# Optimization experiments

Measured on AMD Instinct MI355X. Metric: run time of the kernel, lower is better.

The kernel has to match this reference:

```python
import jax, jax.numpy as jnp
import numpy as np

EPS = 1e-6

def _rms_norm(x, w):
    # per-head RMSNorm over last dim (head_dim)
    var = jnp.mean(jnp.square(x), axis=-1, keepdims=True)
    return x * jax.lax.rsqrt(var + EPS) * w

def _linear(x, w, b):
    # torch nn.Linear: y = x @ W^T + b
    return jnp.einsum('bsd,od->bso', x, w) + b

def setup_inputs() -> dict:
    key = jax.random.key(0)
    ks = jax.random.split(key, 16)
    B, S, S_enc, D, H, HD = 1, 2048, 256, 1536, 24, 64
    w = lambda k: jax.random.normal(k, (D, D), dtype=jnp.float32) * 0.02
    return {
        'hidden_states': jax.random.normal(ks[0], (B, S, D), dtype=jnp.float32),
        'encoder_hidden_states': jax.random.normal(ks[1], (B, S_enc, D), dtype=jnp.float32),
        'attention_mask': jnp.zeros((B, 1, 1, S + S_enc), dtype=jnp.float32),
        'to_q_weight': w(ks[2]), 'to_q_bias': jnp.zeros((D,), jnp.float32),
        'to_k_weight': w(ks[3]), 'to_k_bias': jnp.zeros((D,), jnp.float32),
        'to_v_weight': w(ks[4]), 'to_v_bias': jnp.zeros((D,), jnp.float32),
        'norm_q_weight': jnp.ones((HD,), jnp.float32),
        'norm_k_weight': jnp.ones((HD,), jnp.float32),
        'add_q_proj_weight': w(ks[5]), 'add_q_proj_bias': jnp.zeros((D,), jnp.float32),
        'add_k_proj_weight': w(ks[6]), 'add_k_proj_bias': jnp.zeros((D,), jnp.float32),
        'add_v_proj_weight': w(ks[7]), 'add_v_proj_bias': jnp.zeros((D,), jnp.float32),
        'norm_added_q_weight': jnp.ones((HD,), jnp.float32),
        'norm_added_k_weight': jnp.ones((HD,), jnp.float32),
        'to_out_0_weight': w(ks[8]), 'to_out_0_bias': jnp.zeros((D,), jnp.float32),
        'to_add_out_weight': w(ks[9]), 'to_add_out_bias': jnp.zeros((D,), jnp.float32),
        'attn_heads': 24,
        'attn_head_dim': 64,
    }

def reference(hidden_states, encoder_hidden_states, attention_mask,
              to_q_weight, to_q_bias, to_k_weight, to_k_bias, to_v_weight, to_v_bias,
              norm_q_weight, norm_k_weight,
              add_q_proj_weight, add_q_proj_bias, add_k_proj_weight, add_k_proj_bias,
              add_v_proj_weight, add_v_proj_bias,
              norm_added_q_weight, norm_added_k_weight,
              to_out_0_weight, to_out_0_bias, to_add_out_weight, to_add_out_bias,
              attn_heads, attn_head_dim):
    B, S, D = hidden_states.shape
    S_enc = encoder_hidden_states.shape[1]
    H, HD = attn_heads, attn_head_dim
    scale = float(HD) ** -0.5

    def split_heads(x):  # [B,T,H*HD] -> [B,H,T,HD]
        return x.reshape(B, -1, H, HD).transpose(0, 2, 1, 3)

    # hidden-stream QKV + per-head RMSNorm on q,k
    q = _rms_norm(split_heads(_linear(hidden_states, to_q_weight, to_q_bias)), norm_q_weight)
    k = _rms_norm(split_heads(_linear(hidden_states, to_k_weight, to_k_bias)), norm_k_weight)
    v = split_heads(_linear(hidden_states, to_v_weight, to_v_bias))

    # encoder-stream QKV + per-head RMSNorm on q,k
    eq = _rms_norm(split_heads(_linear(encoder_hidden_states, add_q_proj_weight, add_q_proj_bias)), norm_added_q_weight)
    ek = _rms_norm(split_heads(_linear(encoder_hidden_states, add_k_proj_weight, add_k_proj_bias)), norm_added_k_weight)
    ev = split_heads(_linear(encoder_hidden_states, add_v_proj_weight, add_v_proj_bias))

    # concat streams along sequence: [B,H,S+S_enc,HD]
    q = jnp.concatenate([q, eq], axis=2)
    k = jnp.concatenate([k, ek], axis=2)
    v = jnp.concatenate([v, ev], axis=2)

    # SDPA with additive mask
    scores = jnp.einsum('bhqd,bhkd->bhqk', q, k) * scale + attention_mask
    probs = jax.nn.softmax(scores, axis=-1)
    out = jnp.einsum('bhqk,bhkd->bhqd', probs, v)  # [B,H,T,HD]
    out = out.transpose(0, 2, 1, 3).reshape(B, S + S_enc, H * HD)

    # split back into image / text streams, separate output projections
    attn_output = _linear(out[:, :S], to_out_0_weight, to_out_0_bias)
    context_attn_output = _linear(out[:, S:], to_add_out_weight, to_add_out_bias)
    del context_attn_output  # AttentionFunc returns only the hidden-stream output
    return attn_output
```

## Files before the change

### kernel.cpp

```cpp
#include <hip/hip_runtime.h>
#include <cstdint>


typedef __attribute__((ext_vector_type(8))) short s16x8;
typedef __attribute__((ext_vector_type(4))) float f32x4;

#define LOG2E 1.4426950408889634f

__device__ __forceinline__ short f2bf(float f) {
  union { float f; uint32_t u; } v; v.f = f;
  uint32_t r = v.u + 0x7FFFu + ((v.u >> 16) & 1u);
  return (short)(r >> 16);
}
__device__ __forceinline__ short f2bf_fast(float f) {
  union { float f; uint32_t u; } v; v.f = f;
  return (short)((v.u + 0x8000u) >> 16);
}

typedef uint32_t __attribute__((address_space(1)))* gas_u32;
typedef uint32_t __attribute__((address_space(3)))* las_u32;

__device__ __forceinline__ void gload_lds16(const short* g, short* l) {
  __builtin_amdgcn_global_load_lds((gas_u32)(g), (las_u32)(l), 16, 0, 0);
}

struct CvtSeg { const float* src; short* dst; int n4; };
struct CvtArgs { CvtSeg s[8]; };

__global__ __launch_bounds__(256) void cvt_bf16_kernel(CvtArgs a) {
  const int stride = gridDim.x * blockDim.x;
  const int tid = blockIdx.x * blockDim.x + threadIdx.x;
  for (int i = 0; i < 8; ++i) {
    const float4* src = (const float4*)a.s[i].src;
    short* dst = a.s[i].dst;
    const int n4 = a.s[i].n4;
    for (int j = tid; j < n4; j += stride) {
      float4 v = src[j];
      short4 o;
      o.x = f2bf(v.x); o.y = f2bf(v.y); o.z = f2bf(v.z); o.w = f2bf(v.w);
      *(short4*)(dst + (size_t)j * 4) = o;
    }
  }
}

enum { MODE_Q = 0, MODE_K = 1, MODE_V = 2, MODE_OUT = 3 };

struct GemmCfg {
  const short* A;
  const short* W;
  const float* bias;
  const float* normw;
  void* dst;
  int toff;
  int mode;
  int mtiles;
};
struct GemmArgs { GemmCfg c[5]; };

__global__ __launch_bounds__(256) void proj_gemm_kernel(GemmArgs args) {
  const GemmCfg cfg = args.c[blockIdx.z];
  if ((int)blockIdx.y >= cfg.mtiles) return;
  constexpr int K = 1536;
  __shared__ short As[4096];
  __shared__ short Bs[4096];
  const int t = threadIdx.x;
  const int lane = t & 63;
  const int wave = t >> 6;
  const int l16 = lane & 15;
  const int quad = lane >> 4;
  const int wm = wave >> 1;
  const int wn = wave & 1;

  const short* __restrict__ Ag = cfg.A + (size_t)(blockIdx.y * 128) * K;
  const short* __restrict__ Wg = cfg.W + (size_t)(blockIdx.x * 128) * K;
  const int srow = t >> 2;
  const int scol = (t & 3) << 3;

  const f32x4 z4 = {0.f, 0.f, 0.f, 0.f};
  f32x4 acc[4][4];
#pragma unroll
  for (int i = 0; i < 4; ++i) {
#pragma unroll
    for (int j = 0; j < 4; ++j) acc[i][j] = z4;
  }

  for (int k0 = 0; k0 < K; k0 += 32) {
    gload_lds16(Ag + (size_t)srow * K + k0 + scol, As + t * 8);
    gload_lds16(Ag + (size_t)(srow + 64) * K + k0 + scol, As + 2048 + t * 8);
    gload_lds16(Wg + (size_t)srow * K + k0 + scol, Bs + t * 8);
    gload_lds16(Wg + (size_t)(srow + 64) * K + k0 + scol, Bs + 2048 + t * 8);
    __syncthreads();
    s16x8 af[4], bfr[4];
#pragma unroll
    for (int i = 0; i < 4; ++i)
      af[i] = *(const s16x8*)(As + (wm * 64 + i * 16 + l16) * 32 + quad * 8);
#pragma unroll
    for (int i = 0; i < 4; ++i)
      bfr[i] = *(const s16x8*)(Bs + (wn * 64 + i * 16 + l16) * 32 + quad * 8);
#pragma unroll
    for (int mi = 0; mi < 4; ++mi) {
#pragma unroll
      for (int ni = 0; ni < 4; ++ni)
        acc[mi][ni] = __builtin_amdgcn_mfma_f32_16x16x32_bf16(af[mi], bfr[ni], acc[mi][ni], 0, 0, 0);
    }
    __syncthreads();
  }

  const int nbase = blockIdx.x * 128 + wn * 64;
  const int mbase = blockIdx.y * 128 + wm * 64;
  const int mode = cfg.mode;
  const int h = nbase >> 6;

  float biasv[4], nwv[4];
#pragma unroll
  for (int ni = 0; ni < 4; ++ni) {
    int col = nbase + ni * 16 + l16;
    biasv[ni] = cfg.bias[col];
    nwv[ni] = (mode == MODE_Q || mode == MODE_K) ? cfg.normw[col & 63] : 0.f;
  }

#pragma unroll
  for (int mi = 0; mi < 4; ++mi) {
    float vv[4][4];
#pragma unroll
    for (int ni = 0; ni < 4; ++ni) {
#pragma unroll
      for (int r = 0; r < 4; ++r) vv[ni][r] = acc[mi][ni][r] + biasv[ni];
    }
    if (mode == MODE_Q || mode == MODE_K) {
      float ss[4];
#pragma unroll
      for (int r = 0; r < 4; ++r)
        ss[r] = vv[0][r] * vv[0][r] + vv[1][r] * vv[1][r] +
                vv[2][r] * vv[2][r] + vv[3][r] * vv[3][r];
#pragma unroll
      for (int r = 0; r < 4; ++r) {
        ss[r] += __shfl_xor(ss[r], 1);
        ss[r] += __shfl_xor(ss[r], 2);
        ss[r] += __shfl_xor(ss[r], 4);
        ss[r] += __shfl_xor(ss[r], 8);
        float rs = rsqrtf(ss[r] * (1.0f / 64.0f) + 1e-6f);
#pragma unroll
        for (int ni = 0; ni < 4; ++ni) vv[ni][r] *= rs * nwv[ni];
      }
    }
    const int row0 = mbase + mi * 16 + quad * 4;
    if (mode == MODE_Q) {
      short* Qd = (short*)cfg.dst;
#pragma unroll
      for (int ni = 0; ni < 4; ++ni) {
        int d = ni * 16 + l16;
#pragma unroll
        for (int r = 0; r < 4; ++r)
          Qd[((size_t)h * 2048 + row0 + r) * 64 + d] = f2bf(vv[ni][r]);
      }
    } else if (mode == MODE_K) {
      short* Kd = (short*)cfg.dst;
#pragma unroll
      for (int ni = 0; ni < 4; ++ni) {
        int d = ni * 16 + l16;
#pragma unroll
        for (int r = 0; r < 4; ++r)
          Kd[((size_t)h * 2304 + cfg.toff + row0 + r) * 64 + d] = f2bf(vv[ni][r]);
      }
    } else if (mode == MODE_V) {
      short* Vd = (short*)cfg.dst;
#pragma unroll
      for (int ni = 0; ni < 4; ++ni) {
        int d = ni * 16 + l16;
        short4 o4;
        o4.x = f2bf(vv[ni][0]); o4.y = f2bf(vv[ni][1]);
        o4.z = f2bf(vv[ni][2]); o4.w = f2bf(vv[ni][3]);
        *(short4*)(Vd + ((size_t)h * 64 + d) * 2304 + cfg.toff + row0) = o4;
      }
    } else {
      float* Od = (float*)cfg.dst;
#pragma unroll
      for (int ni = 0; ni < 4; ++ni) {
        int col = nbase + ni * 16 + l16;
#pragma unroll
        for (int r = 0; r < 4; ++r)
          Od[(size_t)(row0 + r) * 1536 + col] = vv[ni][r];
      }
    }
  }
}

__global__ __launch_bounds__(256) void flash_kernel(
    const short* __restrict__ Q, const short* __restrict__ Kc,
    const short* __restrict__ VT, const float* __restrict__ mask,
    short* __restrict__ AO) {
  const int b = blockIdx.x;
  const int h = (b & 7) * 3 + ((b >> 3) % 3);
  const int q0 = ((b >> 3) / 3) * 64;
  const int lane = threadIdx.x & 63;
  const int wave = threadIdx.x >> 6;
  const int l16 = lane & 15;
  const int quad = lane >> 4;

  __shared__ __align__(16) short smem[20480];
  short* Pw = smem + 16384 + wave * 1024;

  const short* Kh = Kc + (size_t)h * 2304 * 64;
  const short* Vh = VT + (size_t)h * 64 * 2304;

  const short* Qrow = Q + ((size_t)h * 2048 + q0 + wave * 16 + l16) * 64;
  s16x8 aq0 = *(const s16x8*)(Qrow + quad * 8);
  s16x8 aq1 = *(const s16x8*)(Qrow + quad * 8 + 32);

  s16x8 ones;
#pragma unroll
  for (int i = 0; i < 8; ++i) ones[i] = (short)0x3F80;

  const f32x4 z4 = {0.f, 0.f, 0.f, 0.f};
  f32x4 o[4] = {z4, z4, z4, z4};
  f32x4 lacc = z4;
  const float SC = 0.125f * LOG2E;

  const int srow = lane >> 3;
  const int schunk = (lane & 7) ^ srow;

  auto stage = [&](int kb, int buf) {
    const short* kg = Kh + (size_t)(kb + wave * 16) * 64;
    short* kt = smem + buf * 4096 + wave * 1024;
    gload_lds16(kg + srow * 64 + schunk * 8, kt + lane * 8);
    gload_lds16(kg + (srow + 8) * 64 + schunk * 8, kt + 512 + lane * 8);
    const short* vg = Vh + (size_t)(wave * 16 + srow) * 2304 + kb;
    short* vt = smem + 8192 + buf * 4096 + wave * 1024;
    gload_lds16(vg + schunk * 8, vt + lane * 8);
    gload_lds16(vg + (size_t)8 * 2304 + schunk * 8, vt + 512 + lane * 8);
  };

  stage(0, 0);
  __syncthreads();

  for (int it = 0; it < 36; ++it) {
    const int buf = it & 1;
    if (it < 35) stage((it + 1) * 64, buf ^ 1);
    const short* kt = smem + buf * 4096;
    const short* vt = smem + 8192 + buf * 4096;
    const int kb = it * 64;

#pragma unroll
    for (int ni = 0; ni < 4; ++ni) {
      const int r = ni * 16 + l16;
      const short* kr = kt + r * 64;
      s16x8 bk0 = *(const s16x8*)(kr + ((quad ^ (r & 7)) << 3));
      s16x8 bk1 = *(const s16x8*)(kr + (((quad + 4) ^ (r & 7)) << 3));
      f32x4 p0 = __builtin_amdgcn_mfma_f32_16x16x32_bf16(aq0, bk0, z4, 0, 0, 0);
      f32x4 s  = __builtin_amdgcn_mfma_f32_16x16x32_bf16(aq1, bk1, p0, 0, 0, 0);
      float mvl = mask[kb + r] * LOG2E;
      int cb = r >> 3;
#pragma unroll
      for (int rr = 0; rr < 4; ++rr) {
        float pv = __builtin_amdgcn_exp2f(fmaf(s[rr], SC, mvl));
        int prow = quad * 4 + rr;
        Pw[prow * 64 + ((cb ^ (prow & 7)) << 3) + (r & 7)] = f2bf_fast(pv);
      }
    }
    s16x8 ap0 = *(const s16x8*)(Pw + l16 * 64 + ((quad ^ (l16 & 7)) << 3));
    s16x8 ap1 = *(const s16x8*)(Pw + l16 * 64 + (((quad + 4) ^ (l16 & 7)) << 3));
    lacc = __builtin_amdgcn_mfma_f32_16x16x32_bf16(ap0, ones, lacc, 0, 0, 0);
    lacc = __builtin_amdgcn_mfma_f32_16x16x32_bf16(ap1, ones, lacc, 0, 0, 0);
#pragma unroll
    for (int ni = 0; ni < 4; ++ni) {
      const int r = ni * 16 + l16;
      const short* vr = vt + r * 64;
      s16x8 bv0 = *(const s16x8*)(vr + ((quad ^ (r & 7)) << 3));
      s16x8 bv1 = *(const s16x8*)(vr + (((quad + 4) ^ (r & 7)) << 3));
      o[ni] = __builtin_amdgcn_mfma_f32_16x16x32_bf16(ap0, bv0, o[ni], 0, 0, 0);
      o[ni] = __builtin_amdgcn_mfma_f32_16x16x32_bf16(ap1, bv1, o[ni], 0, 0, 0);
    }
    __syncthreads();
  }

#pragma unroll
  for (int rr = 0; rr < 4; ++rr) {
    float inv = 1.0f / lacc[rr];
    int tq = q0 + wave * 16 + quad * 4 + rr;
#pragma unroll
    for (int ni = 0; ni < 4; ++ni)
      AO[(size_t)tq * 1536 + h * 64 + ni * 16 + l16] = f2bf(o[ni][rr] * inv);
  }
}

extern "C" void kernel_launch(void* const* d_in, const int* in_sizes, int n_in,
                              void* d_out, int out_size, void* d_ws, size_t ws_size,
                              hipStream_t stream) {
  (void)in_sizes; (void)n_in; (void)out_size; (void)ws_size;
  const float* hidden = (const float*)d_in[0];
  const float* enc    = (const float*)d_in[1];
  const float* amask  = (const float*)d_in[2];
  const float* wq  = (const float*)d_in[3];  const float* bq  = (const float*)d_in[4];
  const float* wk  = (const float*)d_in[5];  const float* bk  = (const float*)d_in[6];
  const float* wv  = (const float*)d_in[7];  const float* bv  = (const float*)d_in[8];
  const float* nqw = (const float*)d_in[9];  const float* nkw = (const float*)d_in[10];
  const float* wak = (const float*)d_in[13]; const float* bak = (const float*)d_in[14];
  const float* wav = (const float*)d_in[15]; const float* bav = (const float*)d_in[16];
  const float* nakw = (const float*)d_in[18];
  const float* wo  = (const float*)d_in[19]; const float* bo  = (const float*)d_in[20];
  float* out = (float*)d_out;

  char* p = (char*)d_ws;
  auto carve = [&](size_t bytes) { char* r = p; p += (bytes + 255) & ~(size_t)255; return r; };
  short* Xb   = (short*)carve((size_t)2048 * 1536 * 2);
  short* Eb   = (short*)carve((size_t)256 * 1536 * 2);
  short* Wqb  = (short*)carve((size_t)1536 * 1536 * 2);
  short* Wkb  = (short*)carve((size_t)1536 * 1536 * 2);
  short* Wvb  = (short*)carve((size_t)1536 * 1536 * 2);
  short* Wakb = (short*)carve((size_t)1536 * 1536 * 2);
  short* Wavb = (short*)carve((size_t)1536 * 1536 * 2);
  short* Wob  = (short*)carve((size_t)1536 * 1536 * 2);
  short* Qb   = (short*)carve((size_t)24 * 2048 * 64 * 2);
  short* Kb   = (short*)carve((size_t)24 * 2304 * 64 * 2);
  short* VTb  = (short*)carve((size_t)24 * 64 * 2304 * 2);
  short* AOb  = (short*)carve((size_t)2048 * 1536 * 2);

  CvtArgs ca;
  ca.s[0] = {hidden, Xb, 2048 * 1536 / 4};
  ca.s[1] = {enc,    Eb, 256 * 1536 / 4};
  ca.s[2] = {wq,  Wqb,  1536 * 1536 / 4};
  ca.s[3] = {wk,  Wkb,  1536 * 1536 / 4};
  ca.s[4] = {wv,  Wvb,  1536 * 1536 / 4};
  ca.s[5] = {wak, Wakb, 1536 * 1536 / 4};
  ca.s[6] = {wav, Wavb, 1536 * 1536 / 4};
  ca.s[7] = {wo,  Wob,  1536 * 1536 / 4};
  cvt_bf16_kernel<<<dim3(1024), dim3(256), 0, stream>>>(ca);

  GemmArgs g1;
  g1.c[0] = {Xb, Wqb,  bq,  nqw,     (void*)Qb,  0,    MODE_Q, 16};
  g1.c[1] = {Xb, Wkb,  bk,  nkw,     (void*)Kb,  0,    MODE_K, 16};
  g1.c[2] = {Xb, Wvb,  bv,  nullptr, (void*)VTb, 0,    MODE_V, 16};
  g1.c[3] = {Eb, Wakb, bak, nakw,    (void*)Kb,  2048, MODE_K, 2};
  g1.c[4] = {Eb, Wavb, bav, nullptr, (void*)VTb, 2048, MODE_V, 2};
  proj_gemm_kernel<<<dim3(12, 16, 5), dim3(256), 0, stream>>>(g1);

  flash_kernel<<<dim3(768), dim3(256), 0, stream>>>(Qb, Kb, VTb, amask, AOb);

  GemmArgs g3;
  g3.c[0] = {AOb, Wob, bo, nullptr, (void*)out, 0, MODE_OUT, 16};
  proj_gemm_kernel<<<dim3(12, 16, 1), dim3(256), 0, stream>>>(g3);
}
```

Baseline: 304.0 us.

## Split flash attention KV across waves and widen GEMM K-tile with swizzled LDS

The projection GEMM now stages a 64-wide K slice per iteration into LDS with an XOR swizzle, which halves the number of barriers and is meant to reduce LDS bank conflicts. The flash kernel now gives each block 32 query rows instead of 64 and splits the 2304-key range between two wave pairs. Each pair keeps its own partial output and row sum, and the two are combined through shared memory at the end, so the grid doubles to 1536 blocks. The aim is more parallelism and occupancy in attention, paid for by an extra reduction step and by loading each Q tile twice as often relative to the KV traffic.

```diff
diff --git a/kernel.cpp b/kernel.cpp
--- a/kernel.cpp
+++ b/kernel.cpp
@@ -61,8 +61,8 @@
   const GemmCfg cfg = args.c[blockIdx.z];
   if ((int)blockIdx.y >= cfg.mtiles) return;
   constexpr int K = 1536;
-  __shared__ short As[4096];
-  __shared__ short Bs[4096];
+  __shared__ short As[8192];
+  __shared__ short Bs[8192];
   const int t = threadIdx.x;
   const int lane = t & 63;
   const int wave = t >> 6;
@@ -73,8 +73,9 @@
 
   const short* __restrict__ Ag = cfg.A + (size_t)(blockIdx.y * 128) * K;
   const short* __restrict__ Wg = cfg.W + (size_t)(blockIdx.x * 128) * K;
-  const int srow = t >> 2;
-  const int scol = (t & 3) << 3;
+  const int srow = t >> 3;
+  const int cpos = t & 7;
+  const int srcc = cpos ^ (srow & 7);
 
   const f32x4 z4 = {0.f, 0.f, 0.f, 0.f};
   f32x4 acc[4][4];
@@ -84,24 +85,29 @@
     for (int j = 0; j < 4; ++j) acc[i][j] = z4;
   }
 
-  for (int k0 = 0; k0 < K; k0 += 32) {
-    gload_lds16(Ag + (size_t)srow * K + k0 + scol, As + t * 8);
-    gload_lds16(Ag + (size_t)(srow + 64) * K + k0 + scol, As + 2048 + t * 8);
-    gload_lds16(Wg + (size_t)srow * K + k0 + scol, Bs + t * 8);
-    gload_lds16(Wg + (size_t)(srow + 64) * K + k0 + scol, Bs + 2048 + t * 8);
+  for (int k0 = 0; k0 < K; k0 += 64) {
+#pragma unroll
+    for (int j = 0; j < 4; ++j) {
+      const size_t roff = (size_t)(j * 32 + srow) * K + k0 + srcc * 8;
+      gload_lds16(Ag + roff, As + j * 2048 + t * 8);
+      gload_lds16(Wg + roff, Bs + j * 2048 + t * 8);
+    }
     __syncthreads();
-    s16x8 af[4], bfr[4];
-#pragma unroll
-    for (int i = 0; i < 4; ++i)
-      af[i] = *(const s16x8*)(As + (wm * 64 + i * 16 + l16) * 32 + quad * 8);
-#pragma unroll
-    for (int i = 0; i < 4; ++i)
-      bfr[i] = *(const s16x8*)(Bs + (wn * 64 + i * 16 + l16) * 32 + quad * 8);
-#pragma unroll
-    for (int mi = 0; mi < 4; ++mi) {
-#pragma unroll
-      for (int ni = 0; ni < 4; ++ni)
-        acc[mi][ni] = __builtin_amdgcn_mfma_f32_16x16x32_bf16(af[mi], bfr[ni], acc[mi][ni], 0, 0, 0);
+#pragma unroll
+    for (int kh = 0; kh < 2; ++kh) {
+      s16x8 af[4], bfr[4];
+#pragma unroll
+      for (int i = 0; i < 4; ++i) {
+        int pos = (kh * 4 + quad) ^ (l16 & 7);
+        af[i]  = *(const s16x8*)(As + (wm * 64 + i * 16 + l16) * 64 + pos * 8);
+        bfr[i] = *(const s16x8*)(Bs + (wn * 64 + i * 16 + l16) * 64 + pos * 8);
+      }
+#pragma unroll
+      for (int mi = 0; mi < 4; ++mi) {
+#pragma unroll
+        for (int ni = 0; ni < 4; ++ni)
+          acc[mi][ni] = __builtin_amdgcn_mfma_f32_16x16x32_bf16(af[mi], bfr[ni], acc[mi][ni], 0, 0, 0);
+      }
     }
     __syncthreads();
   }
@@ -192,19 +198,21 @@
     short* __restrict__ AO) {
   const int b = blockIdx.x;
   const int h = (b & 7) * 3 + ((b >> 3) % 3);
-  const int q0 = ((b >> 3) / 3) * 64;
+  const int q0 = ((b >> 3) / 3) * 32;
   const int lane = threadIdx.x & 63;
   const int wave = threadIdx.x >> 6;
+  const int qw = wave & 1;
+  const int ks = wave >> 1;
   const int l16 = lane & 15;
   const int quad = lane >> 4;
 
-  __shared__ __align__(16) short smem[20480];
-  short* Pw = smem + 16384 + wave * 1024;
+  __shared__ __align__(16) short smem[18432];
+  short* Pw = smem + 16384 + wave * 512;
 
   const short* Kh = Kc + (size_t)h * 2304 * 64;
   const short* Vh = VT + (size_t)h * 64 * 2304;
 
-  const short* Qrow = Q + ((size_t)h * 2048 + q0 + wave * 16 + l16) * 64;
+  const short* Qrow = Q + ((size_t)h * 2048 + q0 + qw * 16 + l16) * 64;
   s16x8 aq0 = *(const s16x8*)(Qrow + quad * 8);
   s16x8 aq1 = *(const s16x8*)(Qrow + quad * 8 + 32);
 
@@ -216,19 +224,22 @@
   f32x4 o[4] = {z4, z4, z4, z4};
   f32x4 lacc = z4;
   const float SC = 0.125f * LOG2E;
-
-  const int srow = lane >> 3;
-  const int schunk = (lane & 7) ^ srow;
-
-  auto stage = [&](int kb, int buf) {
-    const short* kg = Kh + (size_t)(kb + wave * 16) * 64;
-    short* kt = smem + buf * 4096 + wave * 1024;
-    gload_lds16(kg + srow * 64 + schunk * 8, kt + lane * 8);
-    gload_lds16(kg + (srow + 8) * 64 + schunk * 8, kt + 512 + lane * 8);
-    const short* vg = Vh + (size_t)(wave * 16 + srow) * 2304 + kb;
-    short* vt = smem + 8192 + buf * 4096 + wave * 1024;
-    gload_lds16(vg + schunk * 8, vt + lane * 8);
-    gload_lds16(vg + (size_t)8 * 2304 + schunk * 8, vt + 512 + lane * 8);
+  const int kbase = ks * 1152;
+
+  auto stage = [&](int it, int buf) {
+    const int kb = kbase + it * 32;
+    short* kt = smem + (ks * 2 + buf) * 2048;
+    short* vt = smem + 8192 + (ks * 2 + buf) * 2048;
+#pragma unroll
+    for (int c = 0; c < 2; ++c) {
+      int s = c * 128 + qw * 64 + lane;
+      int trow = s >> 3, cp = s & 7;
+      gload_lds16(Kh + (size_t)(kb + trow) * 64 + (cp ^ (trow & 7)) * 8,
+                  kt + c * 1024 + qw * 512 + lane * 8);
+      int d = s >> 2, cpv = s & 3;
+      gload_lds16(Vh + (size_t)d * 2304 + kb + ((cpv ^ ((d >> 1) & 3)) * 8),
+                  vt + c * 1024 + qw * 512 + lane * 8);
+    }
   };
 
   stage(0, 0);
@@ -236,51 +247,60 @@
 
   for (int it = 0; it < 36; ++it) {
     const int buf = it & 1;
-    if (it < 35) stage((it + 1) * 64, buf ^ 1);
-    const short* kt = smem + buf * 4096;
-    const short* vt = smem + 8192 + buf * 4096;
-    const int kb = it * 64;
-
-#pragma unroll
-    for (int ni = 0; ni < 4; ++ni) {
-      const int r = ni * 16 + l16;
-      const short* kr = kt + r * 64;
-      s16x8 bk0 = *(const s16x8*)(kr + ((quad ^ (r & 7)) << 3));
-      s16x8 bk1 = *(const s16x8*)(kr + (((quad + 4) ^ (r & 7)) << 3));
+    if (it < 35) stage(it + 1, buf ^ 1);
+    const short* kt = smem + (ks * 2 + buf) * 2048;
+    const short* vt = smem + 8192 + (ks * 2 + buf) * 2048;
+    const int kb = kbase + it * 32;
+
+#pragma unroll
+    for (int ni = 0; ni < 2; ++ni) {
+      const int tt = ni * 16 + l16;
+      const short* kr = kt + tt * 64;
+      s16x8 bk0 = *(const s16x8*)(kr + ((quad ^ (tt & 7)) << 3));
+      s16x8 bk1 = *(const s16x8*)(kr + (((quad + 4) ^ (tt & 7)) << 3));
       f32x4 p0 = __builtin_amdgcn_mfma_f32_16x16x32_bf16(aq0, bk0, z4, 0, 0, 0);
       f32x4 s  = __builtin_amdgcn_mfma_f32_16x16x32_bf16(aq1, bk1, p0, 0, 0, 0);
-      float mvl = mask[kb + r] * LOG2E;
-      int cb = r >> 3;
+      float mvl = mask[kb + tt] * LOG2E;
+      const int cc = tt >> 3;
 #pragma unroll
       for (int rr = 0; rr < 4; ++rr) {
         float pv = __builtin_amdgcn_exp2f(fmaf(s[rr], SC, mvl));
         int prow = quad * 4 + rr;
-        Pw[prow * 64 + ((cb ^ (prow & 7)) << 3) + (r & 7)] = f2bf_fast(pv);
-      }
-    }
-    s16x8 ap0 = *(const s16x8*)(Pw + l16 * 64 + ((quad ^ (l16 & 7)) << 3));
-    s16x8 ap1 = *(const s16x8*)(Pw + l16 * 64 + (((quad + 4) ^ (l16 & 7)) << 3));
-    lacc = __builtin_amdgcn_mfma_f32_16x16x32_bf16(ap0, ones, lacc, 0, 0, 0);
-    lacc = __builtin_amdgcn_mfma_f32_16x16x32_bf16(ap1, ones, lacc, 0, 0, 0);
+        Pw[prow * 32 + ((cc ^ ((prow >> 1) & 3)) << 3) + (tt & 7)] = f2bf_fast(pv);
+      }
+    }
+    s16x8 ap = *(const s16x8*)(Pw + l16 * 32 + ((quad ^ ((l16 >> 1) & 3)) << 3));
+    lacc = __builtin_amdgcn_mfma_f32_16x16x32_bf16(ap, ones, lacc, 0, 0, 0);
 #pragma unroll
     for (int ni = 0; ni < 4; ++ni) {
-      const int r = ni * 16 + l16;
-      const short* vr = vt + r * 64;
-      s16x8 bv0 = *(const s16x8*)(vr + ((quad ^ (r & 7)) << 3));
-      s16x8 bv1 = *(const s16x8*)(vr + (((quad + 4) ^ (r & 7)) << 3));
-      o[ni] = __builtin_amdgcn_mfma_f32_16x16x32_bf16(ap0, bv0, o[ni], 0, 0, 0);
-      o[ni] = __builtin_amdgcn_mfma_f32_16x16x32_bf16(ap1, bv1, o[ni], 0, 0, 0);
+      const int d = ni * 16 + l16;
+      s16x8 bv = *(const s16x8*)(vt + d * 32 + ((quad ^ ((d >> 1) & 3)) << 3));
+      o[ni] = __builtin_amdgcn_mfma_f32_16x16x32_bf16(ap, bv, o[ni], 0, 0, 0);
     }
     __syncthreads();
   }
 
-#pragma unroll
-  for (int rr = 0; rr < 4; ++rr) {
-    float inv = 1.0f / lacc[rr];
-    int tq = q0 + wave * 16 + quad * 4 + rr;
-#pragma unroll
-    for (int ni = 0; ni < 4; ++ni)
-      AO[(size_t)tq * 1536 + h * 64 + ni * 16 + l16] = f2bf(o[ni][rr] * inv);
+  f32x4* R = (f32x4*)smem;
+  if (ks == 1) {
+    f32x4* Rw = R + (qw * 64 + lane) * 5;
+#pragma unroll
+    for (int ni = 0; ni < 4; ++ni) Rw[ni] = o[ni];
+    Rw[4] = lacc;
+  }
+  __syncthreads();
+  if (ks == 0) {
+    const f32x4* Rw = R + (qw * 64 + lane) * 5;
+#pragma unroll
+    for (int ni = 0; ni < 4; ++ni) o[ni] += Rw[ni];
+    lacc += Rw[4];
+#pragma unroll
+    for (int rr = 0; rr < 4; ++rr) {
+      float inv = 1.0f / lacc[rr];
+      int tq = q0 + qw * 16 + quad * 4 + rr;
+#pragma unroll
+      for (int ni = 0; ni < 4; ++ni)
+        AO[(size_t)tq * 1536 + h * 64 + ni * 16 + l16] = f2bf(o[ni][rr] * inv);
+    }
   }
 }
 
@@ -335,7 +355,7 @@
   g1.c[4] = {Eb, Wavb, bav, nullptr, (void*)VTb, 2048, MODE_V, 2};
   proj_gemm_kernel<<<dim3(12, 16, 5), dim3(256), 0, stream>>>(g1);
 
-  flash_kernel<<<dim3(768), dim3(256), 0, stream>>>(Qb, Kb, VTb, amask, AOb);
+  flash_kernel<<<dim3(1536), dim3(256), 0, stream>>>(Qb, Kb, VTb, amask, AOb);
 
   GemmArgs g3;
   g3.c[0] = {AOb, Wob, bo, nullptr, (void*)out, 0, MODE_OUT, 16};
```

Measured after the change: 325.6 us. 7.1% more time.
